# Optimization experiments

Hardware: AMD Instinct MI355X
Metric: run time of the kernel (lower is better)

Reference implementation:

```python
import jax, jax.numpy as jnp
import numpy as np

HIDDEN = 1024
HEADS = 16
HEAD_DIM = HIDDEN // HEADS
SCALE = 1.0 / (HEAD_DIM ** 0.5)


def setup_inputs() -> dict:
    key = jax.random.key(0)
    k1, k2, k3 = jax.random.split(key, 3)
    B, S = 2, 2048
    x = jax.random.normal(k1, (B, S, HIDDEN), dtype=jnp.float32)
    # torch Linear weights: (out_features, in_features), y = x @ W.T
    qkv_w = jax.random.normal(k2, (3 * HIDDEN, HIDDEN), dtype=jnp.float32) * (HIDDEN ** -0.5)
    out_w = jax.random.normal(k3, (HIDDEN, HIDDEN), dtype=jnp.float32) * (HIDDEN ** -0.5)
    return {"x": x, "qkv_w": qkv_w, "out_w": out_w}


def reference(x, qkv_w, out_w):
    B, S, H = x.shape
    qkv = jnp.einsum('bsh,oh->bso', x, qkv_w)  # [B,S,3H]
    q, k, v = jnp.split(qkv, 3, axis=-1)
    def heads(t):
        return t.reshape(B, S, HEADS, HEAD_DIM).transpose(0, 2, 1, 3)  # [B,nh,S,hd]
    q, k, v = heads(q), heads(k), heads(v)
    scores = jnp.einsum('bhqd,bhkd->bhqk', q, k) * SCALE  # [B,nh,S,S]
    attn = jax.nn.softmax(scores, axis=-1)
    out = jnp.einsum('bhqk,bhkd->bhqd', attn, v)  # [B,nh,S,hd]
    out = out.transpose(0, 2, 1, 3).reshape(B, S, H)
    return jnp.einsum('bsh,oh->bso', out, out_w)
```

## Files before the change

kernel.cpp:

```cpp
#include <hip/hip_runtime.h>
#include <hip/hip_bf16.h>

#define BB 2
#define SS 2048
#define HH 1024
#define NH 16
#define HD 64
#define MM (BB * SS)
#define N_QKV (3 * HH)
#define KK HH

typedef __attribute__((ext_vector_type(8))) short short8;
typedef __attribute__((ext_vector_type(4))) float floatx4;
typedef __attribute__((ext_vector_type(16))) float floatx16;

#define MFMA16(a, b, c) __builtin_amdgcn_mfma_f32_16x16x32_bf16(a, b, c, 0, 0, 0)
#define MFMA32(a, b, c) __builtin_amdgcn_mfma_f32_32x32x16_bf16(a, b, c, 0, 0, 0)

__device__ __forceinline__ unsigned short f2bf(float f) {
  unsigned int u = __builtin_bit_cast(unsigned int, f);
  u += 0x7FFFu + ((u >> 16) & 1u);
  return (unsigned short)(u >> 16);
}

__device__ __forceinline__ float fexp2(float x) {
#if __has_builtin(__builtin_amdgcn_exp2f)
  return __builtin_amdgcn_exp2f(x);
#else
  float r; asm("v_exp_f32 %0, %1" : "=v"(r) : "v"(x)); return r;
#endif
}

__device__ __forceinline__ unsigned int pack2(float lo, float hi) {
  unsigned int a = __builtin_bit_cast(unsigned int, lo) + 0x8000u;
  unsigned int b = __builtin_bit_cast(unsigned int, hi) + 0x8000u;
  return __builtin_amdgcn_perm(b, a, 0x07060302u);
}

#define N4X (MM * HH / 4)
#define N4Q (N_QKV * KK / 4)
#define N4O (HH * KK / 4)
__global__ __launch_bounds__(256) void cast3_f32_bf16(const float* __restrict__ x,
                                                      const float* __restrict__ qw,
                                                      const float* __restrict__ ow,
                                                      unsigned short* __restrict__ xb,
                                                      unsigned short* __restrict__ qwb,
                                                      unsigned short* __restrict__ owb) {
  int i = blockIdx.x * blockDim.x + threadIdx.x;
  const float* src; unsigned short* dst; int idx;
  if (i < N4X) { src = x; dst = xb; idx = i; }
  else if (i < N4X + N4Q) { src = qw; dst = qwb; idx = i - N4X; }
  else { src = ow; dst = owb; idx = i - N4X - N4Q; }
  float4 f = ((const float4*)src)[idx];
  ushort4 u;
  u.x = f2bf(f.x); u.y = f2bf(f.y); u.z = f2bf(f.z); u.w = f2bf(f.w);
  ((ushort4*)dst)[idx] = u;
}

__global__ __launch_bounds__(256) void gemm_qkv(const unsigned short* __restrict__ A,
                                                const unsigned short* __restrict__ W,
                                                unsigned short* __restrict__ qb,
                                                unsigned short* __restrict__ kb,
                                                unsigned short* __restrict__ vtb) {
  __shared__ __attribute__((aligned(16))) unsigned short As[128 * 32];
  __shared__ __attribute__((aligned(16))) unsigned short Bs[128 * 32];
  const int tid = threadIdx.x;
  const int wave = tid >> 6, lane = tid & 63;
  const int quad = lane >> 4, lc = lane & 15;
  const int m0 = blockIdx.y * 128, n0 = blockIdx.x * 128;
  const int wm = (wave >> 1) * 64, wn = (wave & 1) * 64;

  floatx4 acc[4][4];
#pragma unroll
  for (int i = 0; i < 4; i++)
#pragma unroll
    for (int j = 0; j < 4; j++) acc[i][j] = (floatx4){0.f, 0.f, 0.f, 0.f};

  const unsigned short* Ag = A + (size_t)(m0 + (tid >> 2)) * KK + (tid & 3) * 8;
  const unsigned short* Bg = W + (size_t)(n0 + (tid >> 2)) * KK + (tid & 3) * 8;
  unsigned short* AsW = As + wave * 512 + lane * 8;
  unsigned short* BsW = Bs + wave * 512 + lane * 8;

  uint4 a0 = *(const uint4*)(Ag);
  uint4 a1 = *(const uint4*)(Ag + (size_t)64 * KK);
  uint4 b0 = *(const uint4*)(Bg);
  uint4 b1 = *(const uint4*)(Bg + (size_t)64 * KK);

  for (int it = 0; it < KK / 32; ++it) {
    __syncthreads();
    *(uint4*)(AsW) = a0;
    *(uint4*)(AsW + 2048) = a1;
    *(uint4*)(BsW) = b0;
    *(uint4*)(BsW + 2048) = b1;
    if (it + 1 < KK / 32) {
      int k0 = (it + 1) * 32;
      a0 = *(const uint4*)(Ag + k0);
      a1 = *(const uint4*)(Ag + k0 + (size_t)64 * KK);
      b0 = *(const uint4*)(Bg + k0);
      b1 = *(const uint4*)(Bg + k0 + (size_t)64 * KK);
    }
    __syncthreads();
    short8 af[4], bf[4];
#pragma unroll
    for (int i = 0; i < 4; i++) {
      af[i] = *(const short8*)(As + (wm + i * 16 + lc) * 32 + quad * 8);
      bf[i] = *(const short8*)(Bs + (wn + i * 16 + lc) * 32 + quad * 8);
    }
#pragma unroll
    for (int i = 0; i < 4; i++)
#pragma unroll
      for (int j = 0; j < 4; j++) acc[i][j] = MFMA16(af[i], bf[j], acc[i][j]);
  }

  const float QSCALE = 0.125f * 1.44269504f;
#pragma unroll
  for (int j = 0; j < 4; j++) {
    int n = n0 + wn + j * 16 + lc;
#pragma unroll
    for (int i = 0; i < 4; i++) {
      int mbase = m0 + wm + i * 16 + quad * 4;
      int b = mbase >> 11;
      int s0 = mbase & 2047;
      if (n < HH) {
        int h = n >> 6, d = n & 63;
#pragma unroll
        for (int r = 0; r < 4; r++)
          qb[(((size_t)(b * NH + h) * SS + s0 + r) * HD) + d] = f2bf(acc[i][j][r] * QSCALE);
      } else if (n < 2 * HH) {
        int n2 = n - HH; int h = n2 >> 6, d = n2 & 63;
#pragma unroll
        for (int r = 0; r < 4; r++)
          kb[(((size_t)(b * NH + h) * SS + s0 + r) * HD) + d] = f2bf(acc[i][j][r]);
      } else {
        int n2 = n - 2 * HH; int h = n2 >> 6, d = n2 & 63;
        ushort4 p;
        p.x = f2bf(acc[i][j][0]); p.y = f2bf(acc[i][j][1]);
        p.z = f2bf(acc[i][j][2]); p.w = f2bf(acc[i][j][3]);
        *(ushort4*)(vtb + ((size_t)(b * NH + h) * HD + d) * SS + s0) = p;
      }
    }
  }
}

__device__ __forceinline__ int co(int row, int c16) {
  return row * 64 + ((c16 ^ ((row ^ (row >> 3)) & 7)) << 3);
}

__global__ __launch_bounds__(256, 2) void attn_kernel(const unsigned short* __restrict__ qg,
                                                      const unsigned short* __restrict__ kg,
                                                      const unsigned short* __restrict__ vtg,
                                                      unsigned short* __restrict__ og) {
  __shared__ __attribute__((aligned(16))) unsigned short Sall[16384];
  unsigned short* Qs = Sall;
  unsigned short* Ks = Sall + 8192;
  unsigned short* Vs = Sall + 12288;

  const int tid = threadIdx.x;
  const int w = tid >> 6, lane = tid & 63;
  const int hl = lane >> 5, c = lane & 31;
  const int q0 = blockIdx.x * 128;
  const int head = blockIdx.y, b = blockIdx.z;

  const unsigned short* qbase = qg + (size_t)(b * NH + head) * SS * HD;
  const unsigned short* kbase = kg + (size_t)(b * NH + head) * SS * HD;
  const unsigned short* vbase = vtg + (size_t)(b * NH + head) * HD * SS;

  {
    int row = tid >> 3, cc = tid & 7;
#pragma unroll
    for (int s = 0; s < 4; s++)
      *(uint4*)(Qs + co(row + 32 * s, cc)) =
          *(const uint4*)(qbase + (size_t)(q0 + row + 32 * s) * HD + cc * 8);
  }

  const int frow = tid >> 3, fc = tid & 7;
  uint4 k0r = *(const uint4*)(kbase + (size_t)frow * HD + fc * 8);
  uint4 k1r = *(const uint4*)(kbase + (size_t)(frow + 32) * HD + fc * 8);
  uint4 v0r = *(const uint4*)(vbase + (size_t)frow * SS + fc * 8);
  uint4 v1r = *(const uint4*)(vbase + (size_t)(frow + 32) * SS + fc * 8);

  floatx16 oacc0, oacc1, lacc;
#pragma unroll
  for (int i = 0; i < 16; i++) { oacc0[i] = 0.f; oacc1[i] = 0.f; lacc[i] = 0.f; }

  short8 ones;
#pragma unroll
  for (int i = 0; i < 8; i++) ones[i] = (short)0x3F80;

  short8 qa[4];

  for (int kt = 0; kt < SS; kt += 64) {
    __syncthreads();
    *(uint4*)(Ks + co(frow, fc)) = k0r;
    *(uint4*)(Ks + co(frow + 32, fc)) = k1r;
    *(uint4*)(Vs + co(frow, fc)) = v0r;
    *(uint4*)(Vs + co(frow + 32, fc)) = v1r;
    if (kt + 64 < SS) {
      k0r = *(const uint4*)(kbase + (size_t)(kt + 64 + frow) * HD + fc * 8);
      k1r = *(const uint4*)(kbase + (size_t)(kt + 96 + frow) * HD + fc * 8);
      v0r = *(const uint4*)(vbase + (size_t)frow * SS + kt + 64 + fc * 8);
      v1r = *(const uint4*)(vbase + (size_t)(frow + 32) * SS + kt + 64 + fc * 8);
    }
    __syncthreads();

    if (kt == 0) {
#pragma unroll
      for (int ks = 0; ks < 4; ks++)
        qa[ks] = *(const short8*)(Qs + co(w * 32 + c, ks * 2 + hl));
    }

    floatx16 sacc0, sacc1;
#pragma unroll
    for (int i = 0; i < 16; i++) { sacc0[i] = 0.f; sacc1[i] = 0.f; }
#pragma unroll
    for (int ks = 0; ks < 4; ks++) {
      short8 ka0 = *(const short8*)(Ks + co(c, ks * 2 + hl));
      short8 ka1 = *(const short8*)(Ks + co(32 + c, ks * 2 + hl));
      sacc0 = MFMA32(ka0, qa[ks], sacc0);
      sacc1 = MFMA32(ka1, qa[ks], sacc1);
    }

    short8 pb[4];
#pragma unroll
    for (int kb = 0; kb < 4; kb++) {
      const floatx16& s = (kb < 2) ? sacc0 : sacc1;
      int base = (kb & 1) * 8;
      unsigned int u0 = pack2(fexp2(s[base + 0]), fexp2(s[base + 1]));
      unsigned int u1 = pack2(fexp2(s[base + 2]), fexp2(s[base + 3]));
      unsigned int u2 = pack2(fexp2(s[base + 4]), fexp2(s[base + 5]));
      unsigned int u3 = pack2(fexp2(s[base + 6]), fexp2(s[base + 7]));
      uint4 u = {u0, u1, u2, u3};
      pb[kb] = __builtin_bit_cast(short8, u);
    }

#pragma unroll
    for (int kb = 0; kb < 4; kb++) {
      uint2 lo0 = *(const uint2*)(Vs + co(c, 2 * kb) + 4 * hl);
      uint2 hi0 = *(const uint2*)(Vs + co(c, 2 * kb + 1) + 4 * hl);
      uint4 a0 = {lo0.x, lo0.y, hi0.x, hi0.y};
      short8 va0 = __builtin_bit_cast(short8, a0);
      uint2 lo1 = *(const uint2*)(Vs + co(32 + c, 2 * kb) + 4 * hl);
      uint2 hi1 = *(const uint2*)(Vs + co(32 + c, 2 * kb + 1) + 4 * hl);
      uint4 a1 = {lo1.x, lo1.y, hi1.x, hi1.y};
      short8 va1 = __builtin_bit_cast(short8, a1);
      oacc0 = MFMA32(va0, pb[kb], oacc0);
      oacc1 = MFMA32(va1, pb[kb], oacc1);
      lacc = MFMA32(ones, pb[kb], lacc);
    }
  }

  __syncthreads();
  unsigned short* sc = Sall + w * 2176;
  float inv = 1.0f / lacc[0];
#pragma unroll
  for (int t = 0; t < 8; t++) {
    int d0 = ((2 * t) & 3) + 8 * (t >> 1) + 4 * hl;
    *(unsigned int*)(sc + c * 68 + d0) = pack2(oacc0[2 * t] * inv, oacc0[2 * t + 1] * inv);
    *(unsigned int*)(sc + c * 68 + 32 + d0) = pack2(oacc1[2 * t] * inv, oacc1[2 * t + 1] * inv);
  }
  {
    int ql = lane >> 1, hf = lane & 1;
    size_t row = (size_t)(b * SS + q0 + w * 32 + ql);
    unsigned short* dst = og + row * HH + head * 64 + hf * 32;
    const unsigned short* srcp = sc + ql * 68 + hf * 32;
#pragma unroll
    for (int s = 0; s < 4; s++) {
      uint2 a = *(const uint2*)(srcp + s * 8);
      uint2 bq = *(const uint2*)(srcp + s * 8 + 4);
      uint4 v = {a.x, a.y, bq.x, bq.y};
      *(uint4*)(dst + s * 8) = v;
    }
  }
}

__global__ __launch_bounds__(256) void gemm_out(const unsigned short* __restrict__ A,
                                                const unsigned short* __restrict__ W,
                                                float* __restrict__ C) {
  __shared__ __attribute__((aligned(16))) unsigned short As[128 * 32];
  __shared__ __attribute__((aligned(16))) unsigned short Bs[64 * 32];
  const int tid = threadIdx.x;
  const int wave = tid >> 6, lane = tid & 63;
  const int quad = lane >> 4, lc = lane & 15;
  const int m0 = blockIdx.y * 128, n0 = blockIdx.x * 64;
  const int wm = (wave >> 1) * 64, wn = (wave & 1) * 32;

  floatx4 acc[4][2];
#pragma unroll
  for (int i = 0; i < 4; i++)
#pragma unroll
    for (int j = 0; j < 2; j++) acc[i][j] = (floatx4){0.f, 0.f, 0.f, 0.f};

  const unsigned short* Ag = A + (size_t)(m0 + (tid >> 2)) * KK + (tid & 3) * 8;
  const unsigned short* Bg = W + (size_t)(n0 + (tid >> 2)) * KK + (tid & 3) * 8;
  unsigned short* AsW = As + wave * 512 + lane * 8;
  unsigned short* BsW = Bs + wave * 512 + lane * 8;

  uint4 a0 = *(const uint4*)(Ag);
  uint4 a1 = *(const uint4*)(Ag + (size_t)64 * KK);
  uint4 b0 = *(const uint4*)(Bg);

  for (int it = 0; it < KK / 32; ++it) {
    __syncthreads();
    *(uint4*)(AsW) = a0;
    *(uint4*)(AsW + 2048) = a1;
    *(uint4*)(BsW) = b0;
    if (it + 1 < KK / 32) {
      int k0 = (it + 1) * 32;
      a0 = *(const uint4*)(Ag + k0);
      a1 = *(const uint4*)(Ag + k0 + (size_t)64 * KK);
      b0 = *(const uint4*)(Bg + k0);
    }
    __syncthreads();
    short8 af[4], bf[2];
#pragma unroll
    for (int i = 0; i < 4; i++)
      af[i] = *(const short8*)(As + (wm + i * 16 + lc) * 32 + quad * 8);
#pragma unroll
    for (int j = 0; j < 2; j++)
      bf[j] = *(const short8*)(Bs + (wn + j * 16 + lc) * 32 + quad * 8);
#pragma unroll
    for (int i = 0; i < 4; i++)
#pragma unroll
      for (int j = 0; j < 2; j++) acc[i][j] = MFMA16(af[i], bf[j], acc[i][j]);
  }

#pragma unroll
  for (int i = 0; i < 4; i++)
#pragma unroll
    for (int j = 0; j < 2; j++) {
      int m = m0 + wm + i * 16 + quad * 4;
      int n = n0 + wn + j * 16 + lc;
#pragma unroll
      for (int r = 0; r < 4; r++) C[(size_t)(m + r) * HH + n] = acc[i][j][r];
    }
}

extern "C" void kernel_launch(void* const* d_in, const int* in_sizes, int n_in,
                              void* d_out, int out_size, void* d_ws, size_t ws_size,
                              hipStream_t stream) {
  const float* x = (const float*)d_in[0];
  const float* qkv_w = (const float*)d_in[1];
  const float* out_w = (const float*)d_in[2];
  float* out = (float*)d_out;

  char* ws = (char*)d_ws;
  unsigned short* x_bf   = (unsigned short*)(ws + 0);
  unsigned short* qkw_bf = (unsigned short*)(ws + 8388608);
  unsigned short* otw_bf = (unsigned short*)(ws + 14680064);
  unsigned short* qb     = (unsigned short*)(ws + 16777216);
  unsigned short* kb     = (unsigned short*)(ws + 25165824);
  unsigned short* vtb    = (unsigned short*)(ws + 33554432);
  unsigned short* ao     = (unsigned short*)(ws + 41943040);

  cast3_f32_bf16<<<dim3((N4X + N4Q + N4O) / 256), dim3(256), 0, stream>>>(
      x, qkv_w, out_w, x_bf, qkw_bf, otw_bf);
  gemm_qkv<<<dim3(N_QKV / 128, MM / 128), dim3(256), 0, stream>>>(x_bf, qkw_bf, qb, kb, vtb);
  attn_kernel<<<dim3(SS / 128, NH, BB), dim3(256), 0, stream>>>(qb, kb, vtb, ao);
  gemm_out<<<dim3(HH / 64, MM / 128), dim3(256), 0, stream>>>(ao, otw_bf, out);
}
```

Before: 193.2 us.

## Fuse fp32-to-bf16 casts into GEMM tile loads and drop cast kernel

Removes the separate cast kernel and has both GEMMs load fp32 activations and weights directly, converting to bf16 with round-to-nearest-even before the shared-memory store. This saves one launch and the write-then-read of the bf16 copies. In exchange, each GEMM tile now reads twice the global bytes and repeats the conversion for every tile that reuses the same rows. The cheaper truncation-style pack is kept only for the attention paths.

Measured after the change: 190.0 us. Within noise of the previous version (-1.7%).

```diff
diff --git a/kernel.cpp b/kernel.cpp
--- a/kernel.cpp
+++ b/kernel.cpp
@@ -32,33 +32,30 @@
 }
 
 __device__ __forceinline__ unsigned int pack2(float lo, float hi) {
+  unsigned int a = __builtin_bit_cast(unsigned int, lo);
+  unsigned int b = __builtin_bit_cast(unsigned int, hi);
+  a += 0x7FFFu + ((a >> 16) & 1u);
+  b += 0x7FFFu + ((b >> 16) & 1u);
+  return __builtin_amdgcn_perm(b, a, 0x07060302u);
+}
+
+__device__ __forceinline__ unsigned int pack2e(float lo, float hi) {
   unsigned int a = __builtin_bit_cast(unsigned int, lo) + 0x8000u;
   unsigned int b = __builtin_bit_cast(unsigned int, hi) + 0x8000u;
   return __builtin_amdgcn_perm(b, a, 0x07060302u);
 }
 
-#define N4X (MM * HH / 4)
-#define N4Q (N_QKV * KK / 4)
-#define N4O (HH * KK / 4)
-__global__ __launch_bounds__(256) void cast3_f32_bf16(const float* __restrict__ x,
-                                                      const float* __restrict__ qw,
-                                                      const float* __restrict__ ow,
-                                                      unsigned short* __restrict__ xb,
-                                                      unsigned short* __restrict__ qwb,
-                                                      unsigned short* __restrict__ owb) {
-  int i = blockIdx.x * blockDim.x + threadIdx.x;
-  const float* src; unsigned short* dst; int idx;
-  if (i < N4X) { src = x; dst = xb; idx = i; }
-  else if (i < N4X + N4Q) { src = qw; dst = qwb; idx = i - N4X; }
-  else { src = ow; dst = owb; idx = i - N4X - N4Q; }
-  float4 f = ((const float4*)src)[idx];
-  ushort4 u;
-  u.x = f2bf(f.x); u.y = f2bf(f.y); u.z = f2bf(f.z); u.w = f2bf(f.w);
-  ((ushort4*)dst)[idx] = u;
-}
-
-__global__ __launch_bounds__(256) void gemm_qkv(const unsigned short* __restrict__ A,
-                                                const unsigned short* __restrict__ W,
+__device__ __forceinline__ uint4 cvt8(float4 lo, float4 hi) {
+  uint4 u;
+  u.x = pack2(lo.x, lo.y);
+  u.y = pack2(lo.z, lo.w);
+  u.z = pack2(hi.x, hi.y);
+  u.w = pack2(hi.z, hi.w);
+  return u;
+}
+
+__global__ __launch_bounds__(256) void gemm_qkv(const float* __restrict__ X,
+                                                const float* __restrict__ Wf,
                                                 unsigned short* __restrict__ qb,
                                                 unsigned short* __restrict__ kb,
                                                 unsigned short* __restrict__ vtb) {
@@ -76,28 +73,28 @@
 #pragma unroll
     for (int j = 0; j < 4; j++) acc[i][j] = (floatx4){0.f, 0.f, 0.f, 0.f};
 
-  const unsigned short* Ag = A + (size_t)(m0 + (tid >> 2)) * KK + (tid & 3) * 8;
-  const unsigned short* Bg = W + (size_t)(n0 + (tid >> 2)) * KK + (tid & 3) * 8;
+  const float* Ag = X + (size_t)(m0 + (tid >> 2)) * KK + (tid & 3) * 8;
+  const float* Bg = Wf + (size_t)(n0 + (tid >> 2)) * KK + (tid & 3) * 8;
   unsigned short* AsW = As + wave * 512 + lane * 8;
   unsigned short* BsW = Bs + wave * 512 + lane * 8;
 
-  uint4 a0 = *(const uint4*)(Ag);
-  uint4 a1 = *(const uint4*)(Ag + (size_t)64 * KK);
-  uint4 b0 = *(const uint4*)(Bg);
-  uint4 b1 = *(const uint4*)(Bg + (size_t)64 * KK);
+  float4 a0l = *(const float4*)(Ag),                     a0h = *(const float4*)(Ag + 4);
+  float4 a1l = *(const float4*)(Ag + (size_t)64 * KK),   a1h = *(const float4*)(Ag + (size_t)64 * KK + 4);
+  float4 b0l = *(const float4*)(Bg),                     b0h = *(const float4*)(Bg + 4);
+  float4 b1l = *(const float4*)(Bg + (size_t)64 * KK),   b1h = *(const float4*)(Bg + (size_t)64 * KK + 4);
 
   for (int it = 0; it < KK / 32; ++it) {
     __syncthreads();
-    *(uint4*)(AsW) = a0;
-    *(uint4*)(AsW + 2048) = a1;
-    *(uint4*)(BsW) = b0;
-    *(uint4*)(BsW + 2048) = b1;
+    *(uint4*)(AsW) = cvt8(a0l, a0h);
+    *(uint4*)(AsW + 2048) = cvt8(a1l, a1h);
+    *(uint4*)(BsW) = cvt8(b0l, b0h);
+    *(uint4*)(BsW + 2048) = cvt8(b1l, b1h);
     if (it + 1 < KK / 32) {
       int k0 = (it + 1) * 32;
-      a0 = *(const uint4*)(Ag + k0);
-      a1 = *(const uint4*)(Ag + k0 + (size_t)64 * KK);
-      b0 = *(const uint4*)(Bg + k0);
-      b1 = *(const uint4*)(Bg + k0 + (size_t)64 * KK);
+      a0l = *(const float4*)(Ag + k0);                    a0h = *(const float4*)(Ag + k0 + 4);
+      a1l = *(const float4*)(Ag + k0 + (size_t)64 * KK);  a1h = *(const float4*)(Ag + k0 + (size_t)64 * KK + 4);
+      b0l = *(const float4*)(Bg + k0);                    b0h = *(const float4*)(Bg + k0 + 4);
+      b1l = *(const float4*)(Bg + k0 + (size_t)64 * KK);  b1h = *(const float4*)(Bg + k0 + (size_t)64 * KK + 4);
     }
     __syncthreads();
     short8 af[4], bf[4];
@@ -225,10 +222,10 @@
     for (int kb = 0; kb < 4; kb++) {
       const floatx16& s = (kb < 2) ? sacc0 : sacc1;
       int base = (kb & 1) * 8;
-      unsigned int u0 = pack2(fexp2(s[base + 0]), fexp2(s[base + 1]));
-      unsigned int u1 = pack2(fexp2(s[base + 2]), fexp2(s[base + 3]));
-      unsigned int u2 = pack2(fexp2(s[base + 4]), fexp2(s[base + 5]));
-      unsigned int u3 = pack2(fexp2(s[base + 6]), fexp2(s[base + 7]));
+      unsigned int u0 = pack2e(fexp2(s[base + 0]), fexp2(s[base + 1]));
+      unsigned int u1 = pack2e(fexp2(s[base + 2]), fexp2(s[base + 3]));
+      unsigned int u2 = pack2e(fexp2(s[base + 4]), fexp2(s[base + 5]));
+      unsigned int u3 = pack2e(fexp2(s[base + 6]), fexp2(s[base + 7]));
       uint4 u = {u0, u1, u2, u3};
       pb[kb] = __builtin_bit_cast(short8, u);
     }
@@ -255,8 +252,8 @@
 #pragma unroll
   for (int t = 0; t < 8; t++) {
     int d0 = ((2 * t) & 3) + 8 * (t >> 1) + 4 * hl;
-    *(unsigned int*)(sc + c * 68 + d0) = pack2(oacc0[2 * t] * inv, oacc0[2 * t + 1] * inv);
-    *(unsigned int*)(sc + c * 68 + 32 + d0) = pack2(oacc1[2 * t] * inv, oacc1[2 * t + 1] * inv);
+    *(unsigned int*)(sc + c * 68 + d0) = pack2e(oacc0[2 * t] * inv, oacc0[2 * t + 1] * inv);
+    *(unsigned int*)(sc + c * 68 + 32 + d0) = pack2e(oacc1[2 * t] * inv, oacc1[2 * t + 1] * inv);
   }
   {
     int ql = lane >> 1, hf = lane & 1;
@@ -274,7 +271,7 @@
 }
 
 __global__ __launch_bounds__(256) void gemm_out(const unsigned short* __restrict__ A,
-                                                const unsigned short* __restrict__ W,
+                                                const float* __restrict__ Wf,
                                                 float* __restrict__ C) {
   __shared__ __attribute__((aligned(16))) unsigned short As[128 * 32];
   __shared__ __attribute__((aligned(16))) unsigned short Bs[64 * 32];
@@ -291,24 +288,25 @@
     for (int j = 0; j < 2; j++) acc[i][j] = (floatx4){0.f, 0.f, 0.f, 0.f};
 
   const unsigned short* Ag = A + (size_t)(m0 + (tid >> 2)) * KK + (tid & 3) * 8;
-  const unsigned short* Bg = W + (size_t)(n0 + (tid >> 2)) * KK + (tid & 3) * 8;
+  const float* Bg = Wf + (size_t)(n0 + (tid >> 2)) * KK + (tid & 3) * 8;
   unsigned short* AsW = As + wave * 512 + lane * 8;
   unsigned short* BsW = Bs + wave * 512 + lane * 8;
 
   uint4 a0 = *(const uint4*)(Ag);
   uint4 a1 = *(const uint4*)(Ag + (size_t)64 * KK);
-  uint4 b0 = *(const uint4*)(Bg);
+  float4 b0l = *(const float4*)(Bg), b0h = *(const float4*)(Bg + 4);
 
   for (int it = 0; it < KK / 32; ++it) {
     __syncthreads();
     *(uint4*)(AsW) = a0;
     *(uint4*)(AsW + 2048) = a1;
-    *(uint4*)(BsW) = b0;
+    *(uint4*)(BsW) = cvt8(b0l, b0h);
     if (it + 1 < KK / 32) {
       int k0 = (it + 1) * 32;
       a0 = *(const uint4*)(Ag + k0);
       a1 = *(const uint4*)(Ag + k0 + (size_t)64 * KK);
-      b0 = *(const uint4*)(Bg + k0);
+      b0l = *(const float4*)(Bg + k0);
+      b0h = *(const float4*)(Bg + k0 + 4);
     }
     __syncthreads();
     short8 af[4], bf[2];
@@ -344,17 +342,12 @@
   float* out = (float*)d_out;
 
   char* ws = (char*)d_ws;
-  unsigned short* x_bf   = (unsigned short*)(ws + 0);
-  unsigned short* qkw_bf = (unsigned short*)(ws + 8388608);
-  unsigned short* otw_bf = (unsigned short*)(ws + 14680064);
-  unsigned short* qb     = (unsigned short*)(ws + 16777216);
-  unsigned short* kb     = (unsigned short*)(ws + 25165824);
-  unsigned short* vtb    = (unsigned short*)(ws + 33554432);
-  unsigned short* ao     = (unsigned short*)(ws + 41943040);
-
-  cast3_f32_bf16<<<dim3((N4X + N4Q + N4O) / 256), dim3(256), 0, stream>>>(
-      x, qkv_w, out_w, x_bf, qkw_bf, otw_bf);
-  gemm_qkv<<<dim3(N_QKV / 128, MM / 128), dim3(256), 0, stream>>>(x_bf, qkw_bf, qb, kb, vtb);
+  unsigned short* qb  = (unsigned short*)(ws + 0);
+  unsigned short* kb  = (unsigned short*)(ws + 8388608);
+  unsigned short* vtb = (unsigned short*)(ws + 16777216);
+  unsigned short* ao  = (unsigned short*)(ws + 25165824);
+
+  gemm_qkv<<<dim3(N_QKV / 128, MM / 128), dim3(256), 0, stream>>>(x, qkv_w, qb, kb, vtb);
   attn_kernel<<<dim3(SS / 128, NH, BB), dim3(256), 0, stream>>>(qb, kb, vtb, ao);
-  gemm_out<<<dim3(HH / 64, MM / 128), dim3(256), 0, stream>>>(ao, otw_bf, out);
-}
+  gemm_out<<<dim3(HH / 64, MM / 128), dim3(256), 0, stream>>>(ao, out_w, out);
+}
```
